# Kernel tuning notes

Measured on AMD Instinct MI355X. Metric: run time of the kernel, lower is better.

The kernel has to match this reference:

```python
import jax, jax.numpy as jnp
import numpy as np

S, B, L = 64, 32, 64          # seq_len (messages), batch (convs), max tokens per message
V, D = 32000, 300             # vocab, embedding dim
H = 512                       # hidden_dim; per-direction message hidden = H//2
F = 16                        # num_game_features
Hh = H // 2


def lstm_dir(x, mask, Wih, Whh, b, reverse=False):
    """Masked (packed-equivalent) LSTM. x:(T,N,D), mask:(T,N) bool.
    Returns h:(T,N,H) with zeros at invalid steps (matches pad_packed_sequence)."""
    if reverse:
        x, mask = x[::-1], mask[::-1]
    N = x.shape[1]
    Hd = Whh.shape[1]
    xg = jnp.einsum('tnd,gd->tng', x, Wih) + b  # (T,N,4H) input gates precomputed

    def step(carry, inp):
        h, c = carry
        xg_t, m = inp
        g = xg_t + h @ Whh.T
        i, f, gg, o = jnp.split(g, 4, axis=-1)
        c_new = jax.nn.sigmoid(f) * c + jax.nn.sigmoid(i) * jnp.tanh(gg)
        h_new = jax.nn.sigmoid(o) * jnp.tanh(c_new)
        m = m[:, None]
        return (jnp.where(m, h_new, h), jnp.where(m, c_new, c)), jnp.where(m, h_new, 0.0)

    init = (jnp.zeros((N, Hd), x.dtype), jnp.zeros((N, Hd), x.dtype))
    _, hs = jax.lax.scan(step, init, (xg, mask))
    if reverse:
        hs = hs[::-1]
    return hs


def setup_inputs() -> dict:
    key = jax.random.key(0)
    ks = jax.random.split(key, 16)
    s = 1.0 / np.sqrt(Hh)
    sc = 1.0 / np.sqrt(H)
    inp = {
        'messages': jax.random.randint(ks[0], (S, B, L), 0, V),
        'game_features': jax.random.normal(ks[1], (S, B, F), jnp.float32),
        'conv_lengths': jax.random.randint(ks[2], (B,), 1, S + 1),
        'E': jax.random.normal(ks[3], (V, D), jnp.float32) * 0.1,  # frozen embedding
        # message bi-LSTM (forward dir)
        'Wih_f': jax.random.uniform(ks[4], (4 * Hh, D), jnp.float32, -s, s),
        'Whh_f': jax.random.uniform(ks[5], (4 * Hh, Hh), jnp.float32, -s, s),
        'b_f': jax.random.uniform(ks[6], (4 * Hh,), jnp.float32, -s, s),
        # message bi-LSTM (backward dir)
        'Wih_b': jax.random.uniform(ks[7], (4 * Hh, D), jnp.float32, -s, s),
        'Whh_b': jax.random.uniform(ks[8], (4 * Hh, Hh), jnp.float32, -s, s),
        'b_b': jax.random.uniform(ks[9], (4 * Hh,), jnp.float32, -s, s),
        # conversation LSTM
        'Wih_c': jax.random.uniform(ks[10], (4 * H, H), jnp.float32, -sc, sc),
        'Whh_c': jax.random.uniform(ks[11], (4 * H, H), jnp.float32, -sc, sc),
        'b_c': jax.random.uniform(ks[12], (4 * H,), jnp.float32, -sc, sc),
        # classifier
        'Wc': jax.random.uniform(ks[13], (H + F,), jnp.float32, -sc, sc),
        'bc': jax.random.uniform(ks[14], (), jnp.float32, -sc, sc),
    }
    return inp


def reference(messages, game_features, conv_lengths, E, Wih_f, Whh_f, b_f,
              Wih_b, Whh_b, b_b, Wih_c, Whh_c, b_c, Wc, bc):
    # ---- message level: all S*B messages in one batched bi-LSTM pass ----
    flat = messages.reshape(S * B, L)                       # (N, L)
    emb = E[flat]                                           # (N, L, D)
    msg_len = jnp.maximum((flat != 0).sum(1), 1)            # clamp(min=1)
    tmask = jnp.arange(L)[:, None] < msg_len[None, :]       # (L, N)
    x = emb.transpose(1, 0, 2)                              # (L, N, D) time-major
    h_fwd = lstm_dir(x, tmask, Wih_f, Whh_f, b_f, reverse=False)
    h_bwd = lstm_dir(x, tmask, Wih_b, Whh_b, b_b, reverse=True)
    h = jnp.concatenate([h_fwd, h_bwd], axis=-1)            # (L, N, H); zeros at pad
    enc = h.max(axis=0)                                     # maxpool incl. zero pads (torch semantics)
    enc = enc.reshape(S, B, H)
    # ---- conversation level ----
    cmask = jnp.arange(S)[:, None] < conv_lengths[None, :]  # (S, B)
    conv_out = lstm_dir(enc, cmask, Wih_c, Whh_c, b_c)      # (S, B, H), zeros past length
    # dropout is identity at inference
    combined = jnp.concatenate([conv_out, game_features], axis=2)  # (S, B, H+F)
    logits = combined @ Wc + bc                             # (S, B)
    return logits
```

## Files before the change

kernel.cpp:

```cpp
#include <hip/hip_runtime.h>
#include <cmath>

#define S_DIM 64
#define B_DIM 32
#define L_DIM 64
#define NMSG  2048
#define D_DIM 300
#define HH    256
#define HC    512
#define F_DIM 16
#define VOCAB 32000

#define OFF_XGV   0u
#define OFF_WHH   32768000u
#define OFF_WPI   33030144u
#define OFF_WCI   33357824u
#define OFF_WCR   33882112u
#define OFF_ENCB  34406400u
#define OFF_HCONV 34930688u
#define OFF_CCONV 34938880u
#define OFF_CO    34955264u
#define OFF_MLEN  36003840u

typedef __attribute__((ext_vector_type(8))) short s8v;
typedef __attribute__((ext_vector_type(4))) float f4v;
#define MFMA(a,b,c) __builtin_amdgcn_mfma_f32_16x16x32_bf16((a),(b),(c),0,0,0)

__device__ __forceinline__ unsigned short f2bf(float x) {
    unsigned u = __float_as_uint(x);
    return (unsigned short)((u + 0x7FFFu + ((u >> 16) & 1u)) >> 16);
}
__device__ __forceinline__ float bf2f(unsigned short u) {
    return __uint_as_float(((unsigned)u) << 16);
}
__device__ __forceinline__ float sigm(float x) { return 1.0f / (1.0f + __expf(-x)); }
__device__ __forceinline__ float tanh_f(float x) { return 1.0f - 2.0f / (1.0f + __expf(2.0f * x)); }

__device__ __forceinline__ void gload16(const unsigned short* g, unsigned short* l) {
    __builtin_amdgcn_global_load_lds(
        (const __attribute__((address_space(1))) unsigned int*)g,
        (__attribute__((address_space(3))) unsigned int*)l, 16, 0, 0);
}

__global__ __launch_bounds__(256) void pack_whh(
    const float* __restrict__ Whh_f, const float* __restrict__ Whh_b,
    unsigned short* __restrict__ Wp)
{
    int wv = blockIdx.x >> 3, kt = blockIdx.x & 7, dir = blockIdx.y;
    const float* W = dir ? Whh_b : Whh_f;
    int tid = threadIdx.x, lane = tid & 63, iq = tid >> 6;
    int n_l = lane & 15;
    int k0 = kt * 32 + (lane >> 4) * 8;
    #pragma unroll
    for (int ii = 0; ii < 2; ++ii) {
        int i = iq * 2 + ii;
        int nt = (i >> 1) * 16 + wv * 2 + (i & 1);
        int n = nt * 16 + n_l;
        unsigned short tmp[8];
        #pragma unroll
        for (int u = 0; u < 8; ++u) tmp[u] = f2bf(W[(size_t)n * HH + k0 + u]);
        *(uint4*)(Wp + ((size_t)((dir * 8 + wv) * 8 + kt) * 8 + i) * 512 + lane * 8) = *(uint4*)tmp;
    }
}

__global__ __launch_bounds__(256) void pack_wih(
    const float* __restrict__ Wih_f, const float* __restrict__ Wih_b,
    unsigned short* __restrict__ wpi)
{
    int nt = blockIdx.x, dir = blockIdx.y;
    const float* W = dir ? Wih_b : Wih_f;
    int tid = threadIdx.x, lane = tid & 63, ktq = tid >> 6;
    int n = nt * 16 + (lane & 15);
    int kb = (lane >> 4) * 8;
    for (int kt = ktq; kt < 10; kt += 4) {
        int k0 = kt * 32 + kb;
        unsigned short tmp[8];
        #pragma unroll
        for (int u = 0; u < 8; ++u) {
            int k = k0 + u;
            tmp[u] = (k < D_DIM) ? f2bf(W[(size_t)n * D_DIM + k]) : (unsigned short)0;
        }
        *(uint4*)(wpi + (size_t)dir * 327680 + ((size_t)(nt * 10 + kt)) * 512 + lane * 8) = *(uint4*)tmp;
    }
}

__global__ __launch_bounds__(256) void pack_whc(
    const float* __restrict__ Wih_c, const float* __restrict__ Whh_c,
    unsigned short* __restrict__ whci, unsigned short* __restrict__ whcr)
{
    int nt = blockIdx.x, which = blockIdx.y;
    const float* W = which ? Whh_c : Wih_c;
    unsigned short* dst = which ? whcr : whci;
    int tid = threadIdx.x, lane = tid & 63;
    int row = nt * 16 + (lane & 15);
    int kb = (lane >> 4) * 8;
    for (int kt = tid >> 6; kt < 16; kt += 4) {
        int k0 = kt * 32 + kb;
        unsigned short tmp[8];
        #pragma unroll
        for (int u = 0; u < 8; ++u) tmp[u] = f2bf(W[(size_t)row * HC + k0 + u]);
        *(uint4*)(dst + ((size_t)(nt * 16 + kt)) * 512 + lane * 8) = *(uint4*)tmp;
    }
}

__global__ __launch_bounds__(256) void msg_len_kernel(const int* __restrict__ msgs,
                                                      int* __restrict__ mlen) {
    int n = blockIdx.x * 256 + threadIdx.x;
    if (n >= NMSG) return;
    int cnt = 0;
    #pragma unroll 8
    for (int l = 0; l < L_DIM; ++l) cnt += (msgs[n * L_DIM + l] != 0);
    mlen[n] = max(cnt, 1);
}

__global__ __launch_bounds__(256) void init_conv(float* __restrict__ ws) {
    unsigned i = blockIdx.x * 256u + threadIdx.x;
    if (i < 24576u) ws[OFF_HCONV + i] = 0.0f;
}

#define EROW 328
__global__ __launch_bounds__(256) void xg_gemm(
    const float* __restrict__ E,
    const float* __restrict__ b_f, const float* __restrict__ b_b,
    const unsigned short* __restrict__ wpi,
    unsigned short* __restrict__ xgv)
{
    __shared__ __align__(16) unsigned short e_lds[32 * EROW];
    const int w0 = blockIdx.x * 32;
    const int dirb = blockIdx.y;
    const float* bias = dirb ? b_b : b_f;

    const int tid = threadIdx.x, lane = tid & 63, wv = tid >> 6;
    const int l15 = lane & 15, kg = lane >> 4;

    {
        const float4* E4 = (const float4*)(E + (size_t)w0 * D_DIM);
        for (int i = tid; i < 32 * 75; i += 256) {
            int r = i / 75, c = i - r * 75;
            float4 v = E4[r * 75 + c];
            unsigned short t4[4] = { f2bf(v.x), f2bf(v.y), f2bf(v.z), f2bf(v.w) };
            *(uint2*)&e_lds[r * EROW + c * 4] = *(uint2*)t4;
        }
        for (int i = tid; i < 32 * 20; i += 256) {
            int r = i / 20, c = i - r * 20;
            e_lds[r * EROW + 300 + c] = 0;
        }
    }
    __syncthreads();

    s8v a0q[10], a1q[10];
    #pragma unroll
    for (int kt = 0; kt < 10; ++kt) {
        a0q[kt] = *(const s8v*)&e_lds[l15 * EROW + kt * 32 + kg * 8];
        a1q[kt] = *(const s8v*)&e_lds[(16 + l15) * EROW + kt * 32 + kg * 8];
    }

    const unsigned short* wb = wpi + (size_t)dirb * 327680;
    const f4v zf = {0.0f, 0.0f, 0.0f, 0.0f};

    #pragma unroll
    for (int jt = 0; jt < 4; ++jt) {
        f4v acc[2][4];
        #pragma unroll
        for (int m = 0; m < 2; ++m)
            #pragma unroll
            for (int g = 0; g < 4; ++g) acc[m][g] = zf;

        #pragma unroll
        for (int kt = 0; kt < 10; ++kt) {
            #pragma unroll
            for (int g = 0; g < 4; ++g) {
                int nt = g * 16 + jt * 4 + wv;
                s8v b = *(const s8v*)(wb + ((size_t)(nt * 10 + kt)) * 512 + lane * 8);
                acc[0][g] = MFMA(a0q[kt], b, acc[0][g]);
                acc[1][g] = MFMA(a1q[kt], b, acc[1][g]);
            }
        }

        const int j = jt * 64 + wv * 16 + l15;
        float bv[4];
        #pragma unroll
        for (int g = 0; g < 4; ++g) bv[g] = bias[g * 256 + j];
        const int colp = (jt * 2 + (wv >> 1)) * 128 + l15 * 8 + (wv & 1) * 4;
        #pragma unroll
        for (int m = 0; m < 2; ++m)
            #pragma unroll
            for (int r = 0; r < 4; ++r) {
                int w = w0 + m * 16 + kg * 4 + r;
                unsigned short t4[4];
                #pragma unroll
                for (int g = 0; g < 4; ++g) t4[g] = f2bf(acc[m][g][r] + bv[g]);
                *(uint2*)(xgv + ((size_t)dirb * VOCAB + w) * 1024 + colp) = *(uint2*)t4;
            }
    }
}

#define XGS  1032
#define HROW 264
__global__ __launch_bounds__(512, 2) void word_lstm(
    const int* __restrict__ msgs, const int* __restrict__ mlen,
    const unsigned short* __restrict__ xgv,
    const unsigned short* __restrict__ whh,
    unsigned short* __restrict__ enc_bf)
{
    __shared__ __align__(16) unsigned short xg_lds[2][16 * XGS];
    __shared__ __align__(16) unsigned short h_lds[2][16 * HROW];
    __shared__ int tok_s[16 * 64];
    __shared__ int len_s[16];

    const int mg = blockIdx.x >> 1, dir = blockIdx.x & 1;
    const int tid = threadIdx.x, lane = tid & 63, wv = tid >> 6;
    const int l15 = lane & 15, kg = lane >> 4;

    for (int i = tid; i < 16 * 64; i += 512) tok_s[i] = msgs[mg * 1024 + i];
    if (tid < 16) len_s[tid] = mlen[mg * 16 + tid];
    for (int i = tid; i < 2 * 16 * HROW; i += 512) h_lds[0][i] = 0;
    __syncthreads();

    const unsigned short* xv = xgv + (size_t)dir * VOCAB * 1024;

    const unsigned short* wbase = whh + (size_t)(dir * 8 + wv) * 32768 + lane * 8;
    const unsigned short* bp[16];
    #pragma unroll
    for (int jj = 0; jj < 16; ++jj) bp[jj] = wbase + jj * 2048;

    int lens[4];
    #pragma unroll
    for (int r = 0; r < 4; ++r) lens[r] = len_s[kg * 4 + r];

    int bmax = 1;
    #pragma unroll
    for (int i = 0; i < 16; ++i) bmax = max(bmax, len_s[i]);

    float c_st[2][4], rm[2][4];
    unsigned short hbf[2][4];
    #pragma unroll
    for (int q = 0; q < 2; ++q)
        #pragma unroll
        for (int r = 0; r < 4; ++r) { c_st[q][r] = 0.0f; rm[q][r] = -INFINITY; hbf[q][r] = 0; }

    #pragma unroll
    for (int rr = 0; rr < 2; ++rr) {
        int row = wv * 2 + rr;
        int tt = dir ? (len_s[row] - 1) : 0;
        if (tt < 0) tt = 0;
        const unsigned short* src = xv + (size_t)tok_s[row * 64 + tt] * 1024 + lane * 8;
        gload16(src,       &xg_lds[0][row * XGS]);
        gload16(src + 512, &xg_lds[0][row * XGS + 512]);
    }

    for (int t = 0; t < bmax; ++t) {
        __syncthreads();
        const int buf = t & 1;
        const int hbuf = t & 1;

        if (t + 1 < bmax) {
            #pragma unroll
            for (int rr = 0; rr < 2; ++rr) {
                int row = wv * 2 + rr;
                int tn = t + 1;
                int tt = dir ? (len_s[row] - 1 - tn) : tn;
                if (tt < 0) tt = 0;
                const unsigned short* src = xv + (size_t)tok_s[row * 64 + tt] * 1024 + lane * 8;
                gload16(src,       &xg_lds[buf ^ 1][row * XGS]);
                gload16(src + 512, &xg_lds[buf ^ 1][row * XGS + 512]);
            }
        }

        f4v acc[2][4];
        {
            s8v v8[4];
            #pragma unroll
            for (int r = 0; r < 4; ++r)
                v8[r] = *(const s8v*)&xg_lds[buf][(kg * 4 + r) * XGS + wv * 128 + l15 * 8];
            #pragma unroll
            for (int q = 0; q < 2; ++q)
                #pragma unroll
                for (int g = 0; g < 4; ++g) {
                    f4v v;
                    #pragma unroll
                    for (int r = 0; r < 4; ++r)
                        v[r] = bf2f((unsigned short)v8[r][q * 4 + g]);
                    acc[q][g] = v;
                }
        }

        #pragma unroll
        for (int kt = 0; kt < 8; ++kt) {
            s8v a = *(const s8v*)&h_lds[hbuf][l15 * HROW + kt * 32 + kg * 8];
            const unsigned short* pA = bp[kt * 2];
            const unsigned short* pB = bp[kt * 2 + 1];
            acc[0][0] = MFMA(a, *(const s8v*)(pA),        acc[0][0]);
            acc[1][0] = MFMA(a, *(const s8v*)(pA + 512),  acc[1][0]);
            acc[0][1] = MFMA(a, *(const s8v*)(pA + 1024), acc[0][1]);
            acc[1][1] = MFMA(a, *(const s8v*)(pA + 1536), acc[1][1]);
            acc[0][2] = MFMA(a, *(const s8v*)(pB),        acc[0][2]);
            acc[1][2] = MFMA(a, *(const s8v*)(pB + 512),  acc[1][2]);
            acc[0][3] = MFMA(a, *(const s8v*)(pB + 1024), acc[0][3]);
            acc[1][3] = MFMA(a, *(const s8v*)(pB + 1536), acc[1][3]);
        }

        #pragma unroll
        for (int q = 0; q < 2; ++q)
            #pragma unroll
            for (int r = 0; r < 4; ++r) {
                float gi = acc[q][0][r], gf = acc[q][1][r], gc = acc[q][2][r], go = acc[q][3][r];
                float cn = sigm(gf) * c_st[q][r] + sigm(gi) * tanh_f(gc);
                float hn = sigm(go) * tanh_f(cn);
                if (t < lens[r]) {
                    c_st[q][r] = cn;
                    rm[q][r] = fmaxf(rm[q][r], hn);
                    hbf[q][r] = f2bf(hn);
                }
                h_lds[hbuf ^ 1][(kg * 4 + r) * HROW + wv * 32 + q * 16 + l15] = hbf[q][r];
            }
    }

    #pragma unroll
    for (int q = 0; q < 2; ++q)
        #pragma unroll
        for (int r = 0; r < 4; ++r) {
            float v = rm[q][r];
            if (lens[r] < 64) v = fmaxf(v, 0.0f);
            enc_bf[(size_t)(mg * 16 + kg * 4 + r) * HC + dir * HH + wv * 32 + q * 16 + l15] = f2bf(v);
        }
}

#define CROW 520
__global__ __launch_bounds__(256) void xgc_gemm(
    const unsigned short* __restrict__ enc_bf,
    const unsigned short* __restrict__ whci,
    const float* __restrict__ b_c,
    unsigned short* __restrict__ xgc)
{
    __shared__ __align__(16) unsigned short e_lds[32 * CROW];
    const int m0 = blockIdx.x * 32;
    const int n0 = blockIdx.y * 256;
    const int tid = threadIdx.x, lane = tid & 63, wv = tid >> 6;
    const int l15 = lane & 15, kg = lane >> 4;

    for (int i = tid; i < 2048; i += 256) {
        int row = i >> 6, u4 = i & 63;
        ((uint4*)&e_lds[row * CROW])[u4] = ((const uint4*)(enc_bf + (size_t)(m0 + row) * HC))[u4];
    }
    __syncthreads();

    const f4v zf = {0.0f, 0.0f, 0.0f, 0.0f};
    f4v acc[2][4];
    #pragma unroll
    for (int m = 0; m < 2; ++m)
        #pragma unroll
        for (int q = 0; q < 4; ++q) acc[m][q] = zf;

    for (int kt = 0; kt < 16; ++kt) {
        s8v a0 = *(const s8v*)&e_lds[l15 * CROW + kt * 32 + kg * 8];
        s8v a1 = *(const s8v*)&e_lds[(16 + l15) * CROW + kt * 32 + kg * 8];
        #pragma unroll
        for (int q = 0; q < 4; ++q) {
            int nt = (n0 >> 4) + wv * 4 + q;
            s8v b = *(const s8v*)(whci + ((size_t)(nt * 16 + kt)) * 512 + lane * 8);
            acc[0][q] = MFMA(a0, b, acc[0][q]);
            acc[1][q] = MFMA(a1, b, acc[1][q]);
        }
    }

    #pragma unroll
    for (int q = 0; q < 4; ++q) {
        int col = n0 + (wv * 4 + q) * 16 + l15;
        float bv = b_c[col];
        #pragma unroll
        for (int m = 0; m < 2; ++m)
            #pragma unroll
            for (int r = 0; r < 4; ++r)
                xgc[(size_t)(m0 + m * 16 + kg * 4 + r) * 2048 + col] = f2bf(acc[m][q][r] + bv);
    }
}

__global__ __launch_bounds__(256) void conv_step(
    const unsigned short* __restrict__ whcr,
    const unsigned short* __restrict__ xgc,
    const int* __restrict__ conv_len,
    unsigned short* __restrict__ h_bf,
    float* __restrict__ c_ws,
    float* __restrict__ co,
    int s)
{
    __shared__ __align__(16) unsigned short xh[32 * CROW];
    __shared__ float gbuf[4][32][16];

    const int tid = threadIdx.x, jb = blockIdx.x;
    const int lane = tid & 63, g = tid >> 6;
    const int l15 = lane & 15, kg = lane >> 4;

    for (int i = tid; i < 2048; i += 256) {
        int row = i >> 6, u4 = i & 63;
        ((uint4*)&xh[row * CROW])[u4] = ((const uint4*)(h_bf + (size_t)row * HC))[u4];
    }
    __syncthreads();

    const int col = g * 512 + jb * 16 + l15;
    f4v acc0, acc1;
    #pragma unroll
    for (int r = 0; r < 4; ++r) {
        acc0[r] = bf2f(xgc[(size_t)(s * B_DIM + kg * 4 + r) * 2048 + col]);
        acc1[r] = bf2f(xgc[(size_t)(s * B_DIM + 16 + kg * 4 + r) * 2048 + col]);
    }

    const int nt = g * 32 + jb;
    for (int kt = 0; kt < 16; ++kt) {
        s8v a0 = *(const s8v*)&xh[l15 * CROW + kt * 32 + kg * 8];
        s8v a1 = *(const s8v*)&xh[(16 + l15) * CROW + kt * 32 + kg * 8];
        s8v b  = *(const s8v*)(whcr + ((size_t)(nt * 16 + kt)) * 512 + lane * 8);
        acc0 = MFMA(a0, b, acc0);
        acc1 = MFMA(a1, b, acc1);
    }

    #pragma unroll
    for (int r = 0; r < 4; ++r) {
        gbuf[g][kg * 4 + r][l15]      = acc0[r];
        gbuf[g][16 + kg * 4 + r][l15] = acc1[r];
    }
    __syncthreads();

    #pragma unroll
    for (int u = 0; u < 2; ++u) {
        int cell = tid + 256 * u;
        int b = cell >> 4, jj = cell & 15;
        int j = jb * 16 + jj;
        bool valid = s < conv_len[b];
        float g_i = gbuf[0][b][jj], g_f = gbuf[1][b][jj];
        float g_c = gbuf[2][b][jj], g_o = gbuf[3][b][jj];
        float cold = c_ws[b * HC + j];
        float cn = sigm(g_f) * cold + sigm(g_i) * tanh_f(g_c);
        float hn = sigm(g_o) * tanh_f(cn);
        float outv = 0.0f;
        if (valid) {
            c_ws[b * HC + j] = cn;
            h_bf[b * HC + j] = f2bf(hn);
            outv = hn;
        }
        co[((size_t)s * B_DIM + b) * HC + j] = outv;
    }
}

__global__ __launch_bounds__(256) void logits_kernel(
    const float* __restrict__ gfeat, const float* __restrict__ Wc, const float* __restrict__ bc,
    const float* __restrict__ co, float* __restrict__ out)
{
    int o = blockIdx.x * 4 + (threadIdx.x >> 6);
    int lane = threadIdx.x & 63;
    const float* row = co + (size_t)o * HC;
    float sum = 0.0f;
    #pragma unroll
    for (int u = 0; u < 8; ++u) sum += row[lane + 64 * u] * Wc[lane + 64 * u];
    if (lane < F_DIM) sum += gfeat[o * F_DIM + lane] * Wc[HC + lane];
    #pragma unroll
    for (int off = 32; off > 0; off >>= 1) sum += __shfl_down(sum, off, 64);
    if (lane == 0) out[o] = sum + bc[0];
}

extern "C" void kernel_launch(void* const* d_in, const int* in_sizes, int n_in,
                              void* d_out, int out_size, void* d_ws, size_t ws_size,
                              hipStream_t stream) {
    const int*   msgs    = (const int*)  d_in[0];
    const float* gfeat   = (const float*)d_in[1];
    const int*   convlen = (const int*)  d_in[2];
    const float* E       = (const float*)d_in[3];
    const float* Wih_f   = (const float*)d_in[4];
    const float* Whh_f   = (const float*)d_in[5];
    const float* b_f     = (const float*)d_in[6];
    const float* Wih_b   = (const float*)d_in[7];
    const float* Whh_b   = (const float*)d_in[8];
    const float* b_b     = (const float*)d_in[9];
    const float* Wih_c   = (const float*)d_in[10];
    const float* Whh_c   = (const float*)d_in[11];
    const float* b_c     = (const float*)d_in[12];
    const float* Wc      = (const float*)d_in[13];
    const float* bc      = (const float*)d_in[14];
    float* out = (float*)d_out;
    float* ws  = (float*)d_ws;

    unsigned short* xgv    = (unsigned short*)(ws + OFF_XGV);
    unsigned short* xgc    = (unsigned short*)(ws + OFF_XGV);
    unsigned short* whh    = (unsigned short*)(ws + OFF_WHH);
    unsigned short* wpi    = (unsigned short*)(ws + OFF_WPI);
    unsigned short* whci   = (unsigned short*)(ws + OFF_WCI);
    unsigned short* whcr   = (unsigned short*)(ws + OFF_WCR);
    unsigned short* enc_bf = (unsigned short*)(ws + OFF_ENCB);
    unsigned short* h_bf   = (unsigned short*)(ws + OFF_HCONV);
    float*          c_ws   = ws + OFF_CCONV;
    float*          co     = ws + OFF_CO;
    int*            mlen   = (int*)(ws + OFF_MLEN);

    pack_whh<<<dim3(64, 2), 256, 0, stream>>>(Whh_f, Whh_b, whh);
    pack_wih<<<dim3(64, 2), 256, 0, stream>>>(Wih_f, Wih_b, wpi);
    pack_whc<<<dim3(128, 2), 256, 0, stream>>>(Wih_c, Whh_c, whci, whcr);
    msg_len_kernel<<<NMSG / 256, 256, 0, stream>>>(msgs, mlen);
    init_conv<<<96, 256, 0, stream>>>(ws);
    xg_gemm<<<dim3(1000, 2), 256, 0, stream>>>(E, b_f, b_b, wpi, xgv);

    word_lstm<<<256, 512, 0, stream>>>(msgs, mlen, xgv, whh, enc_bf);

    xgc_gemm<<<dim3(64, 8), 256, 0, stream>>>(enc_bf, whci, b_c, xgc);

    for (int s = 0; s < S_DIM; ++s)
        conv_step<<<32, 256, 0, stream>>>(whcr, xgc, convlen, h_bf, c_ws, co, s);

    logits_kernel<<<NMSG / 4, 256, 0, stream>>>(gfeat, Wc, bc, co, out);
}
```

Measured before the change: 1.224 ms.

## Fuse conversation LSTM into one cooperative persistent kernel with grid sync

Replaces the 64 per-step conv_step launches, the xgc GEMM and the logits kernel with a single 32-block cooperative kernel. It computes the input-gate GEMM in place, keeps the recurrent weights in registers and cell state in registers, and ping-pongs h buffers through global memory across grid.sync. Logits are built from a game-feature init kernel plus atomicAdd partial dot products per step. The aim is to remove per-step launch overhead and the extra co round trip. The cost is that the input GEMM now runs on only 32 blocks, and atomic ordering makes the sums non-deterministic.

```diff
diff --git a/kernel.cpp b/kernel.cpp
--- a/kernel.cpp
+++ b/kernel.cpp
@@ -1,5 +1,8 @@
 #include <hip/hip_runtime.h>
+#include <hip/hip_cooperative_groups.h>
 #include <cmath>
+
+namespace cg = cooperative_groups;
 
 #define S_DIM 64
 #define B_DIM 32
@@ -17,8 +20,8 @@
 #define OFF_WCI   33357824u
 #define OFF_WCR   33882112u
 #define OFF_ENCB  34406400u
-#define OFF_HCONV 34930688u
-#define OFF_CCONV 34938880u
+#define OFF_HG0   34930688u
+#define OFF_HG1   34938880u
 #define OFF_CO    34955264u
 #define OFF_MLEN  36003840u
 
@@ -115,7 +118,19 @@
 
 __global__ __launch_bounds__(256) void init_conv(float* __restrict__ ws) {
     unsigned i = blockIdx.x * 256u + threadIdx.x;
-    if (i < 24576u) ws[OFF_HCONV + i] = 0.0f;
+    if (i < 24576u) ws[OFF_HG0 + i] = 0.0f;
+}
+
+__global__ __launch_bounds__(256) void logits_init(
+    const float* __restrict__ gfeat, const float* __restrict__ Wc, const float* __restrict__ bc,
+    float* __restrict__ out)
+{
+    int o = blockIdx.x * 256 + threadIdx.x;
+    if (o >= NMSG) return;
+    float s = bc[0];
+    #pragma unroll
+    for (int f = 0; f < F_DIM; ++f) s += gfeat[o * F_DIM + f] * Wc[HC + f];
+    out[o] = s;
 }
 
 #define EROW 328
@@ -327,136 +342,125 @@
 }
 
 #define CROW 520
-__global__ __launch_bounds__(256) void xgc_gemm(
+__global__ __launch_bounds__(256) void conv_coop(
     const unsigned short* __restrict__ enc_bf,
     const unsigned short* __restrict__ whci,
+    const unsigned short* __restrict__ whcr,
     const float* __restrict__ b_c,
-    unsigned short* __restrict__ xgc)
-{
-    __shared__ __align__(16) unsigned short e_lds[32 * CROW];
-    const int m0 = blockIdx.x * 32;
-    const int n0 = blockIdx.y * 256;
-    const int tid = threadIdx.x, lane = tid & 63, wv = tid >> 6;
-    const int l15 = lane & 15, kg = lane >> 4;
-
-    for (int i = tid; i < 2048; i += 256) {
-        int row = i >> 6, u4 = i & 63;
-        ((uint4*)&e_lds[row * CROW])[u4] = ((const uint4*)(enc_bf + (size_t)(m0 + row) * HC))[u4];
-    }
-    __syncthreads();
-
-    const f4v zf = {0.0f, 0.0f, 0.0f, 0.0f};
-    f4v acc[2][4];
-    #pragma unroll
-    for (int m = 0; m < 2; ++m)
-        #pragma unroll
-        for (int q = 0; q < 4; ++q) acc[m][q] = zf;
-
-    for (int kt = 0; kt < 16; ++kt) {
-        s8v a0 = *(const s8v*)&e_lds[l15 * CROW + kt * 32 + kg * 8];
-        s8v a1 = *(const s8v*)&e_lds[(16 + l15) * CROW + kt * 32 + kg * 8];
-        #pragma unroll
-        for (int q = 0; q < 4; ++q) {
-            int nt = (n0 >> 4) + wv * 4 + q;
-            s8v b = *(const s8v*)(whci + ((size_t)(nt * 16 + kt)) * 512 + lane * 8);
-            acc[0][q] = MFMA(a0, b, acc[0][q]);
-            acc[1][q] = MFMA(a1, b, acc[1][q]);
-        }
-    }
-
-    #pragma unroll
-    for (int q = 0; q < 4; ++q) {
-        int col = n0 + (wv * 4 + q) * 16 + l15;
-        float bv = b_c[col];
-        #pragma unroll
-        for (int m = 0; m < 2; ++m)
-            #pragma unroll
-            for (int r = 0; r < 4; ++r)
-                xgc[(size_t)(m0 + m * 16 + kg * 4 + r) * 2048 + col] = f2bf(acc[m][q][r] + bv);
-    }
-}
-
-__global__ __launch_bounds__(256) void conv_step(
-    const unsigned short* __restrict__ whcr,
-    const unsigned short* __restrict__ xgc,
     const int* __restrict__ conv_len,
-    unsigned short* __restrict__ h_bf,
-    float* __restrict__ c_ws,
-    float* __restrict__ co,
-    int s)
-{
+    unsigned short* __restrict__ xgc,
+    unsigned short* __restrict__ hg0,
+    unsigned short* __restrict__ hg1,
+    const float* __restrict__ Wc,
+    float* __restrict__ out)
+{
+    cg::grid_group grid = cg::this_grid();
     __shared__ __align__(16) unsigned short xh[32 * CROW];
     __shared__ float gbuf[4][32][16];
 
-    const int tid = threadIdx.x, jb = blockIdx.x;
-    const int lane = tid & 63, g = tid >> 6;
+    const int jb = blockIdx.x;
+    const int tid = threadIdx.x, lane = tid & 63, g = tid >> 6;
     const int l15 = lane & 15, kg = lane >> 4;
-
-    for (int i = tid; i < 2048; i += 256) {
-        int row = i >> 6, u4 = i & 63;
-        ((uint4*)&xh[row * CROW])[u4] = ((const uint4*)(h_bf + (size_t)row * HC))[u4];
-    }
-    __syncthreads();
-
-    const int col = g * 512 + jb * 16 + l15;
-    f4v acc0, acc1;
-    #pragma unroll
-    for (int r = 0; r < 4; ++r) {
-        acc0[r] = bf2f(xgc[(size_t)(s * B_DIM + kg * 4 + r) * 2048 + col]);
-        acc1[r] = bf2f(xgc[(size_t)(s * B_DIM + 16 + kg * 4 + r) * 2048 + col]);
-    }
-
-    const int nt = g * 32 + jb;
-    for (int kt = 0; kt < 16; ++kt) {
-        s8v a0 = *(const s8v*)&xh[l15 * CROW + kt * 32 + kg * 8];
-        s8v a1 = *(const s8v*)&xh[(16 + l15) * CROW + kt * 32 + kg * 8];
-        s8v b  = *(const s8v*)(whcr + ((size_t)(nt * 16 + kt)) * 512 + lane * 8);
-        acc0 = MFMA(a0, b, acc0);
-        acc1 = MFMA(a1, b, acc1);
-    }
-
-    #pragma unroll
-    for (int r = 0; r < 4; ++r) {
-        gbuf[g][kg * 4 + r][l15]      = acc0[r];
-        gbuf[g][16 + kg * 4 + r][l15] = acc1[r];
-    }
-    __syncthreads();
-
-    #pragma unroll
-    for (int u = 0; u < 2; ++u) {
-        int cell = tid + 256 * u;
-        int b = cell >> 4, jj = cell & 15;
-        int j = jb * 16 + jj;
-        bool valid = s < conv_len[b];
-        float g_i = gbuf[0][b][jj], g_f = gbuf[1][b][jj];
-        float g_c = gbuf[2][b][jj], g_o = gbuf[3][b][jj];
-        float cold = c_ws[b * HC + j];
-        float cn = sigm(g_f) * cold + sigm(g_i) * tanh_f(g_c);
-        float hn = sigm(g_o) * tanh_f(cn);
-        float outv = 0.0f;
-        if (valid) {
-            c_ws[b * HC + j] = cn;
-            h_bf[b * HC + j] = f2bf(hn);
-            outv = hn;
-        }
-        co[((size_t)s * B_DIM + b) * HC + j] = outv;
-    }
-}
-
-__global__ __launch_bounds__(256) void logits_kernel(
-    const float* __restrict__ gfeat, const float* __restrict__ Wc, const float* __restrict__ bc,
-    const float* __restrict__ co, float* __restrict__ out)
-{
-    int o = blockIdx.x * 4 + (threadIdx.x >> 6);
-    int lane = threadIdx.x & 63;
-    const float* row = co + (size_t)o * HC;
-    float sum = 0.0f;
-    #pragma unroll
-    for (int u = 0; u < 8; ++u) sum += row[lane + 64 * u] * Wc[lane + 64 * u];
-    if (lane < F_DIM) sum += gfeat[o * F_DIM + lane] * Wc[HC + lane];
-    #pragma unroll
-    for (int off = 32; off > 0; off >>= 1) sum += __shfl_down(sum, off, 64);
-    if (lane == 0) out[o] = sum + bc[0];
+    const int nt_i = g * 32 + jb;
+    const int mycol = g * 512 + jb * 16 + l15;
+
+    {
+        float bv = b_c[mycol];
+        for (int mt = 0; mt < 64; ++mt) {
+            for (int i = tid; i < 2048; i += 256) {
+                int row = i >> 6, u4 = i & 63;
+                ((uint4*)&xh[row * CROW])[u4] =
+                    ((const uint4*)(enc_bf + (size_t)(mt * 32 + row) * HC))[u4];
+            }
+            __syncthreads();
+            f4v a0 = {bv, bv, bv, bv}, a1 = {bv, bv, bv, bv};
+            for (int kt = 0; kt < 16; ++kt) {
+                s8v e0 = *(const s8v*)&xh[l15 * CROW + kt * 32 + kg * 8];
+                s8v e1 = *(const s8v*)&xh[(16 + l15) * CROW + kt * 32 + kg * 8];
+                s8v b  = *(const s8v*)(whci + ((size_t)(nt_i * 16 + kt)) * 512 + lane * 8);
+                a0 = MFMA(e0, b, a0);
+                a1 = MFMA(e1, b, a1);
+            }
+            #pragma unroll
+            for (int r = 0; r < 4; ++r) {
+                xgc[(size_t)(mt * 32 + kg * 4 + r) * 2048 + mycol]      = f2bf(a0[r]);
+                xgc[(size_t)(mt * 32 + 16 + kg * 4 + r) * 2048 + mycol] = f2bf(a1[r]);
+            }
+            __syncthreads();
+        }
+    }
+
+    const int bA = tid >> 4, jjq = tid & 15;
+    const int lenA = conv_len[bA], lenB = conv_len[16 + bA];
+    const float wcj = Wc[jb * 16 + jjq];
+    float cA = 0.0f, cB = 0.0f;
+    unsigned short hA = 0, hB = 0;
+
+    s8v wr[16];
+    #pragma unroll
+    for (int kt = 0; kt < 16; ++kt)
+        wr[kt] = *(const s8v*)(whcr + ((size_t)(nt_i * 16 + kt)) * 512 + lane * 8);
+
+    for (int s = 0; s < S_DIM; ++s) {
+        const unsigned short* hsrc = (s & 1) ? hg1 : hg0;
+        unsigned short*       hdst = (s & 1) ? hg0 : hg1;
+
+        for (int i = tid; i < 2048; i += 256) {
+            int row = i >> 6, u4 = i & 63;
+            ((uint4*)&xh[row * CROW])[u4] = ((const uint4*)(hsrc + (size_t)row * HC))[u4];
+        }
+        __syncthreads();
+
+        f4v acc0, acc1;
+        #pragma unroll
+        for (int r = 0; r < 4; ++r) {
+            acc0[r] = bf2f(xgc[(size_t)(s * B_DIM + kg * 4 + r) * 2048 + mycol]);
+            acc1[r] = bf2f(xgc[(size_t)(s * B_DIM + 16 + kg * 4 + r) * 2048 + mycol]);
+        }
+        #pragma unroll
+        for (int kt = 0; kt < 16; ++kt) {
+            s8v h0 = *(const s8v*)&xh[l15 * CROW + kt * 32 + kg * 8];
+            s8v h1 = *(const s8v*)&xh[(16 + l15) * CROW + kt * 32 + kg * 8];
+            acc0 = MFMA(h0, wr[kt], acc0);
+            acc1 = MFMA(h1, wr[kt], acc1);
+        }
+        #pragma unroll
+        for (int r = 0; r < 4; ++r) {
+            gbuf[g][kg * 4 + r][l15]      = acc0[r];
+            gbuf[g][16 + kg * 4 + r][l15] = acc1[r];
+        }
+        __syncthreads();
+
+        {
+            float gi = gbuf[0][bA][jjq], gf = gbuf[1][bA][jjq];
+            float gc = gbuf[2][bA][jjq], go = gbuf[3][bA][jjq];
+            float cn = sigm(gf) * cA + sigm(gi) * tanh_f(gc);
+            float hn = sigm(go) * tanh_f(cn);
+            float hval = 0.0f;
+            if (s < lenA) { cA = cn; hA = f2bf(hn); hval = hn; }
+            hdst[(size_t)bA * HC + jb * 16 + jjq] = hA;
+            float p = hval * wcj;
+            #pragma unroll
+            for (int off = 8; off; off >>= 1) p += __shfl_down(p, off, 16);
+            if (jjq == 0 && p != 0.0f) atomicAdd(&out[s * B_DIM + bA], p);
+        }
+        {
+            float gi = gbuf[0][16 + bA][jjq], gf = gbuf[1][16 + bA][jjq];
+            float gc = gbuf[2][16 + bA][jjq], go = gbuf[3][16 + bA][jjq];
+            float cn = sigm(gf) * cB + sigm(gi) * tanh_f(gc);
+            float hn = sigm(go) * tanh_f(cn);
+            float hval = 0.0f;
+            if (s < lenB) { cB = cn; hB = f2bf(hn); hval = hn; }
+            hdst[(size_t)(16 + bA) * HC + jb * 16 + jjq] = hB;
+            float p = hval * wcj;
+            #pragma unroll
+            for (int off = 8; off; off >>= 1) p += __shfl_down(p, off, 16);
+            if (jjq == 0 && p != 0.0f) atomicAdd(&out[s * B_DIM + 16 + bA], p);
+        }
+
+        __threadfence();
+        grid.sync();
+    }
 }
 
 extern "C" void kernel_launch(void* const* d_in, const int* in_sizes, int n_in,
@@ -487,9 +491,8 @@
     unsigned short* whci   = (unsigned short*)(ws + OFF_WCI);
     unsigned short* whcr   = (unsigned short*)(ws + OFF_WCR);
     unsigned short* enc_bf = (unsigned short*)(ws + OFF_ENCB);
-    unsigned short* h_bf   = (unsigned short*)(ws + OFF_HCONV);
-    float*          c_ws   = ws + OFF_CCONV;
-    float*          co     = ws + OFF_CO;
+    unsigned short* hg0    = (unsigned short*)(ws + OFF_HG0);
+    unsigned short* hg1    = (unsigned short*)(ws + OFF_HG1);
     int*            mlen   = (int*)(ws + OFF_MLEN);
 
     pack_whh<<<dim3(64, 2), 256, 0, stream>>>(Whh_f, Whh_b, whh);
@@ -497,14 +500,14 @@
     pack_whc<<<dim3(128, 2), 256, 0, stream>>>(Wih_c, Whh_c, whci, whcr);
     msg_len_kernel<<<NMSG / 256, 256, 0, stream>>>(msgs, mlen);
     init_conv<<<96, 256, 0, stream>>>(ws);
+    logits_init<<<NMSG / 256, 256, 0, stream>>>(gfeat, Wc, bc, out);
     xg_gemm<<<dim3(1000, 2), 256, 0, stream>>>(E, b_f, b_b, wpi, xgv);
 
     word_lstm<<<256, 512, 0, stream>>>(msgs, mlen, xgv, whh, enc_bf);
 
-    xgc_gemm<<<dim3(64, 8), 256, 0, stream>>>(enc_bf, whci, b_c, xgc);
-
-    for (int s = 0; s < S_DIM; ++s)
-        conv_step<<<32, 256, 0, stream>>>(whcr, xgc, convlen, h_bf, c_ws, co, s);
-
-    logits_kernel<<<NMSG / 4, 256, 0, stream>>>(gfeat, Wc, bc, co, out);
-}
+    void* args[] = { (void*)&enc_bf, (void*)&whci, (void*)&whcr, (void*)&b_c,
+                     (void*)&convlen, (void*)&xgc, (void*)&hg0, (void*)&hg1,
+                     (void*)&Wc, (void*)&out };
+    hipLaunchCooperativeKernel((const void*)conv_coop, dim3(32), dim3(256),
+                               args, 0, stream);
+}
```

After: 1.744 ms. +42.4%, slower.
